# Performance work log

Hardware: AMD Instinct MI355X
Metric: run time of the kernel (lower is better)

The kernel has to match this reference:

```python
import jax, jax.numpy as jnp
import numpy as np

SEQ, BZ, DIM = 2048, 16, 1024
NUM_LANG, DICT_LEN = 16, 32000


def setup_inputs() -> dict:
    key = jax.random.key(0)
    ks = jax.random.split(key, 6)
    x = jax.random.normal(ks[0], (SEQ, BZ, DIM), dtype=jnp.float32)
    # raw language ids live at the tail of the dictionary: dict_len-1-raw in [0, num_lang)
    raw = DICT_LEN - 1 - jax.random.randint(ks[1], (BZ,), 0, NUM_LANG)
    W_base = jax.random.normal(ks[2], (DIM, DIM), dtype=jnp.float32) * (DIM ** -0.5)
    b_base = jax.random.normal(ks[3], (DIM,), dtype=jnp.float32) * 0.02
    W = jax.random.uniform(ks[4], (NUM_LANG, DIM, DIM), dtype=jnp.float32) * (DIM ** -0.5)
    bias = jax.random.uniform(ks[5], (NUM_LANG, DIM), dtype=jnp.float32)
    return {"x": x, "lang_ids": raw, "W_base": W_base, "b_base": b_base,
            "W": W, "bias": bias, "dict_len": DICT_LEN, "num_lang": NUM_LANG}


def reference(x, lang_ids, W_base, b_base, W, bias, dict_len, num_lang):
    # Map raw ids to expert indices in [0, num_lang)
    ids = dict_len - 1 - lang_ids                      # [bz]
    # base_model (nn.Linear): h = x @ W_base.T + b_base
    h = jnp.einsum('sbd,ed->sbe', x, W_base) + b_base  # [seq, bz, dim]
    # The original pads each language group to max group size, runs a batched
    # einsum 'abcd,ade->abce' over languages, then scatters back with per-lang
    # bias. Mathematically each batch column j gets W[lang_j] applied:
    We = W[ids]                                        # [bz, dim, dim]
    out = jnp.einsum('sbd,bde->sbe', h, We) + bias[ids][None, :, :]
    return out
```

## Files before the change

kernel.cpp:

```cpp
#include <hip/hip_runtime.h>
#include <stdint.h>

typedef unsigned short u16;
typedef unsigned int u32;
typedef __bf16 bf16x8 __attribute__((ext_vector_type(8)));
typedef float f32x4 __attribute__((ext_vector_type(4)));

#define SEQ 2048
#define BZ 16
#define DIM 1024

__device__ __forceinline__ u16 f2bf(float f) {
    union { float f; u32 u; } a; a.f = f;
    u32 r = a.u + 0x7FFFu + ((a.u >> 16) & 1u);
    return (u16)(r >> 16);
}
__device__ __forceinline__ float bf2f(u16 u) {
    union { u32 u; float f; } a; a.u = ((u32)u) << 16;
    return a.f;
}

__global__ void transpose_cvt(const float* __restrict__ W,
                              const float* __restrict__ W_base,
                              const int* __restrict__ lang_ids,
                              const int* __restrict__ dict_len,
                              u16* __restrict__ Wt,
                              u16* __restrict__ Wbt)
{
    int z = blockIdx.z;
    const float* S;
    u16* D;
    if (z < BZ) {
        int id = dict_len[0] - 1 - lang_ids[z];
        S = W + (size_t)id * DIM * DIM;
        D = Wbt + (size_t)z * DIM * DIM;
    } else {
        S = W_base;
        D = Wt;
    }
    __shared__ float tile[32][33];
    int tx = threadIdx.x, ty = threadIdx.y;
    int x0 = blockIdx.x * 32, y0 = blockIdx.y * 32;
    #pragma unroll
    for (int i = 0; i < 4; i++)
        tile[ty + 8 * i][tx] = S[(size_t)(y0 + ty + 8 * i) * DIM + x0 + tx];
    __syncthreads();
    #pragma unroll
    for (int i = 0; i < 4; i++)
        D[(size_t)(x0 + ty + 8 * i) * DIM + y0 + tx] = f2bf(tile[tx][ty + 8 * i]);
}

__global__ void bb_kernel(const u16* __restrict__ Wbt,
                          const float* __restrict__ b_base,
                          const float* __restrict__ bias,
                          const int* __restrict__ lang_ids,
                          const int* __restrict__ dict_len,
                          float* __restrict__ bb)
{
    int gw = blockIdx.x * 4 + (threadIdx.x >> 6);
    int b = gw >> 10;
    int f = gw & 1023;
    int lane = threadIdx.x & 63;
    const u16* row = Wbt + ((size_t)b * DIM + f) * DIM;
    float s = 0.f;
    #pragma unroll
    for (int i = 0; i < DIM / 64; i++)
        s += bf2f(row[lane + 64 * i]) * b_base[lane + 64 * i];
    #pragma unroll
    for (int off = 32; off; off >>= 1)
        s += __shfl_xor(s, off, 64);
    if (lane == 0) {
        int id = dict_len[0] - 1 - lang_ids[b];
        bb[b * DIM + f] = s + bias[(size_t)id * DIM + f];
    }
}

__global__ void gemm1_kernel(const u16* __restrict__ Wbt,
                             const u16* __restrict__ Wt,
                             u16* __restrict__ CT)
{
    int b = blockIdx.z;
    int f0 = blockIdx.y * 128;
    int d0 = blockIdx.x * 128;
    const u16* A = Wbt + (size_t)b * DIM * DIM;
    const u16* B = Wt;
    u16* C = CT + (size_t)b * DIM * DIM;

    __shared__ u16 As[128 * 32];
    __shared__ u16 Bs[128 * 32];

    int tid = threadIdx.x;
    int wave = tid >> 6, lane = tid & 63;
    int wm = (wave >> 1) * 64, wn = (wave & 1) * 64;
    int quad = lane >> 4, lr = lane & 15;

    f32x4 acc[4][4];
    #pragma unroll
    for (int i = 0; i < 4; i++)
        #pragma unroll
        for (int j = 0; j < 4; j++)
            #pragma unroll
            for (int e = 0; e < 4; e++) acc[i][j][e] = 0.f;

    int r = tid >> 1, c = (tid & 1) * 16;
    for (int k0 = 0; k0 < DIM; k0 += 32) {
        const uint4* asrc = (const uint4*)(A + (size_t)(f0 + r) * DIM + k0 + c);
        const uint4* bsrc = (const uint4*)(B + (size_t)(d0 + r) * DIM + k0 + c);
        uint4 a0 = asrc[0], a1 = asrc[1];
        uint4 b0 = bsrc[0], b1 = bsrc[1];
        *(uint4*)&As[r * 32 + c] = a0;
        *(uint4*)&As[r * 32 + c + 8] = a1;
        *(uint4*)&Bs[r * 32 + c] = b0;
        *(uint4*)&Bs[r * 32 + c + 8] = b1;
        __syncthreads();
        bf16x8 af[4], bfv[4];
        #pragma unroll
        for (int mt = 0; mt < 4; mt++)
            af[mt] = *(const bf16x8*)&As[(wm + mt * 16 + lr) * 32 + quad * 8];
        #pragma unroll
        for (int nt = 0; nt < 4; nt++)
            bfv[nt] = *(const bf16x8*)&Bs[(wn + nt * 16 + lr) * 32 + quad * 8];
        #pragma unroll
        for (int mt = 0; mt < 4; mt++)
            #pragma unroll
            for (int nt = 0; nt < 4; nt++)
                acc[mt][nt] = __builtin_amdgcn_mfma_f32_16x16x32_bf16(
                    af[mt], bfv[nt], acc[mt][nt], 0, 0, 0);
        __syncthreads();
    }
    #pragma unroll
    for (int mt = 0; mt < 4; mt++) {
        int fr = f0 + wm + mt * 16 + quad * 4;
        #pragma unroll
        for (int nt = 0; nt < 4; nt++) {
            int dc = d0 + wn + nt * 16 + lr;
            #pragma unroll
            for (int rr = 0; rr < 4; rr++)
                C[(size_t)(fr + rr) * DIM + dc] = f2bf(acc[mt][nt][rr]);
        }
    }
}

__global__ void gemm2_kernel(const float* __restrict__ x,
                             const u16* __restrict__ CT,
                             const float* __restrict__ bb,
                             float* __restrict__ out)
{
    int b = blockIdx.z;
    int s0 = blockIdx.y * 128;
    int f0 = blockIdx.x * 128;
    const u16* Bm = CT + (size_t)b * DIM * DIM;

    __shared__ u16 As[128 * 32];
    __shared__ u16 Bs[128 * 32];

    int tid = threadIdx.x;
    int wave = tid >> 6, lane = tid & 63;
    int wm = (wave >> 1) * 64, wn = (wave & 1) * 64;
    int quad = lane >> 4, lr = lane & 15;

    f32x4 acc[4][4];
    #pragma unroll
    for (int i = 0; i < 4; i++)
        #pragma unroll
        for (int j = 0; j < 4; j++)
            #pragma unroll
            for (int e = 0; e < 4; e++) acc[i][j][e] = 0.f;

    int r = tid >> 1, c = (tid & 1) * 16;
    for (int k0 = 0; k0 < DIM; k0 += 32) {
        const float4* asrc = (const float4*)(x + ((size_t)(s0 + r) * BZ + b) * DIM + k0 + c);
        float4 fa = asrc[0], fb = asrc[1], fc = asrc[2], fd = asrc[3];
        const uint4* bsrc = (const uint4*)(Bm + (size_t)(f0 + r) * DIM + k0 + c);
        uint4 b0 = bsrc[0], b1 = bsrc[1];
        u32 u0 = f2bf(fa.x) | ((u32)f2bf(fa.y) << 16);
        u32 u1 = f2bf(fa.z) | ((u32)f2bf(fa.w) << 16);
        u32 u2 = f2bf(fb.x) | ((u32)f2bf(fb.y) << 16);
        u32 u3 = f2bf(fb.z) | ((u32)f2bf(fb.w) << 16);
        u32 u4 = f2bf(fc.x) | ((u32)f2bf(fc.y) << 16);
        u32 u5 = f2bf(fc.z) | ((u32)f2bf(fc.w) << 16);
        u32 u6 = f2bf(fd.x) | ((u32)f2bf(fd.y) << 16);
        u32 u7 = f2bf(fd.z) | ((u32)f2bf(fd.w) << 16);
        *(uint4*)&As[r * 32 + c] = make_uint4(u0, u1, u2, u3);
        *(uint4*)&As[r * 32 + c + 8] = make_uint4(u4, u5, u6, u7);
        *(uint4*)&Bs[r * 32 + c] = b0;
        *(uint4*)&Bs[r * 32 + c + 8] = b1;
        __syncthreads();
        bf16x8 af[4], bfv[4];
        #pragma unroll
        for (int mt = 0; mt < 4; mt++)
            af[mt] = *(const bf16x8*)&As[(wm + mt * 16 + lr) * 32 + quad * 8];
        #pragma unroll
        for (int nt = 0; nt < 4; nt++)
            bfv[nt] = *(const bf16x8*)&Bs[(wn + nt * 16 + lr) * 32 + quad * 8];
        #pragma unroll
        for (int mt = 0; mt < 4; mt++)
            #pragma unroll
            for (int nt = 0; nt < 4; nt++)
                acc[mt][nt] = __builtin_amdgcn_mfma_f32_16x16x32_bf16(
                    af[mt], bfv[nt], acc[mt][nt], 0, 0, 0);
        __syncthreads();
    }
    #pragma unroll
    for (int nt = 0; nt < 4; nt++) {
        int fcol = f0 + wn + nt * 16 + lr;
        float bv = bb[b * DIM + fcol];
        #pragma unroll
        for (int mt = 0; mt < 4; mt++) {
            int sr = s0 + wm + mt * 16 + quad * 4;
            #pragma unroll
            for (int rr = 0; rr < 4; rr++)
                out[((size_t)(sr + rr) * BZ + b) * DIM + fcol] = acc[mt][nt][rr] + bv;
        }
    }
}

extern "C" void kernel_launch(void* const* d_in, const int* in_sizes, int n_in,
                              void* d_out, int out_size, void* d_ws, size_t ws_size,
                              hipStream_t stream)
{
    const float* x        = (const float*)d_in[0];
    const int*   lang_ids = (const int*)d_in[1];
    const float* W_base   = (const float*)d_in[2];
    const float* b_base   = (const float*)d_in[3];
    const float* W        = (const float*)d_in[4];
    const float* bias     = (const float*)d_in[5];
    const int*   dict_len = (const int*)d_in[6];
    float* out = (float*)d_out;

    char* ws = (char*)d_ws;
    u16*  Wt  = (u16*)ws;
    u16*  Wbt = (u16*)(ws + (size_t)(2u << 20));
    u16*  CT  = (u16*)(ws + (size_t)(34u << 20));
    float* bb = (float*)(ws + (size_t)(66u << 20));

    transpose_cvt<<<dim3(32, 32, 17), dim3(32, 8, 1), 0, stream>>>(
        W, W_base, lang_ids, dict_len, Wt, Wbt);
    bb_kernel<<<dim3(4096, 1, 1), 256, 0, stream>>>(
        Wbt, b_base, bias, lang_ids, dict_len, bb);
    gemm1_kernel<<<dim3(8, 8, 16), 256, 0, stream>>>(Wbt, Wt, CT);
    gemm2_kernel<<<dim3(8, 16, 16), 256, 0, stream>>>(x, CT, bb, out);
}
```

Before: 481.5 us.

## Pre-convert x to bf16 and use direct global-to-LDS loads in GEMMs

Adds a pass that converts x to bf16 in a batch-major layout up front. Both GEMM kernels now stage tiles with global_load_lds async copies instead of loading through registers and storing to LDS. This removes the per-tile fp32-to-bf16 conversion inside gemm2, which was repeated for every f-tile block, and the extra register round trip. In exchange it costs an extra 128MB read plus 64MB write pass over x and adds a dependence on how the async LDS loads are ordered relative to the barrier.

```diff
diff --git a/kernel.cpp b/kernel.cpp
--- a/kernel.cpp
+++ b/kernel.cpp
@@ -18,6 +18,28 @@
 __device__ __forceinline__ float bf2f(u16 u) {
     union { u32 u; float f; } a; a.u = ((u32)u) << 16;
     return a.f;
+}
+__device__ __forceinline__ void async16(const u16* g, u16* l) {
+    __builtin_amdgcn_global_load_lds(
+        (const __attribute__((address_space(1))) void*)g,
+        (__attribute__((address_space(3))) void*)l, 16, 0, 0);
+}
+
+__global__ void convert_x(const float* __restrict__ x, u16* __restrict__ xb)
+{
+    int s = blockIdx.x;
+    int t = threadIdx.x;
+    const float4* src = (const float4*)(x + (size_t)s * BZ * DIM);
+    #pragma unroll
+    for (int j = 0; j < 16; j++) {
+        int idx = j * 256 + t;
+        float4 v = src[idx];
+        int e = idx * 4;
+        int b = e >> 10, d = e & 1023;
+        u32 lo = f2bf(v.x) | ((u32)f2bf(v.y) << 16);
+        u32 hi = f2bf(v.z) | ((u32)f2bf(v.w) << 16);
+        *(uint2*)(xb + ((size_t)b * SEQ + s) * DIM + d) = make_uint2(lo, hi);
+    }
 }
 
 __global__ void transpose_cvt(const float* __restrict__ W,
@@ -94,6 +116,17 @@
     int wm = (wave >> 1) * 64, wn = (wave & 1) * 64;
     int quad = lane >> 4, lr = lane & 15;
 
+    int srow = wave * 32 + (lane >> 2);
+    int scol = (lane & 3) * 8;
+    const u16* ga0 = A + (size_t)(f0 + srow) * DIM + scol;
+    const u16* ga1 = ga0 + (size_t)16 * DIM;
+    const u16* gb0 = B + (size_t)(d0 + srow) * DIM + scol;
+    const u16* gb1 = gb0 + (size_t)16 * DIM;
+    u16* la0 = &As[(wave * 32) * 32];
+    u16* la1 = &As[(wave * 32 + 16) * 32];
+    u16* lb0 = &Bs[(wave * 32) * 32];
+    u16* lb1 = &Bs[(wave * 32 + 16) * 32];
+
     f32x4 acc[4][4];
     #pragma unroll
     for (int i = 0; i < 4; i++)
@@ -102,16 +135,10 @@
             #pragma unroll
             for (int e = 0; e < 4; e++) acc[i][j][e] = 0.f;
 
-    int r = tid >> 1, c = (tid & 1) * 16;
     for (int k0 = 0; k0 < DIM; k0 += 32) {
-        const uint4* asrc = (const uint4*)(A + (size_t)(f0 + r) * DIM + k0 + c);
-        const uint4* bsrc = (const uint4*)(B + (size_t)(d0 + r) * DIM + k0 + c);
-        uint4 a0 = asrc[0], a1 = asrc[1];
-        uint4 b0 = bsrc[0], b1 = bsrc[1];
-        *(uint4*)&As[r * 32 + c] = a0;
-        *(uint4*)&As[r * 32 + c + 8] = a1;
-        *(uint4*)&Bs[r * 32 + c] = b0;
-        *(uint4*)&Bs[r * 32 + c + 8] = b1;
+        async16(ga0, la0); async16(ga1, la1);
+        async16(gb0, lb0); async16(gb1, lb1);
+        ga0 += 32; ga1 += 32; gb0 += 32; gb1 += 32;
         __syncthreads();
         bf16x8 af[4], bfv[4];
         #pragma unroll
@@ -141,7 +168,7 @@
     }
 }
 
-__global__ void gemm2_kernel(const float* __restrict__ x,
+__global__ void gemm2_kernel(const u16* __restrict__ xb,
                              const u16* __restrict__ CT,
                              const float* __restrict__ bb,
                              float* __restrict__ out)
@@ -149,6 +176,7 @@
     int b = blockIdx.z;
     int s0 = blockIdx.y * 128;
     int f0 = blockIdx.x * 128;
+    const u16* A = xb + (size_t)b * SEQ * DIM;
     const u16* Bm = CT + (size_t)b * DIM * DIM;
 
     __shared__ u16 As[128 * 32];
@@ -159,6 +187,17 @@
     int wm = (wave >> 1) * 64, wn = (wave & 1) * 64;
     int quad = lane >> 4, lr = lane & 15;
 
+    int srow = wave * 32 + (lane >> 2);
+    int scol = (lane & 3) * 8;
+    const u16* ga0 = A + (size_t)(s0 + srow) * DIM + scol;
+    const u16* ga1 = ga0 + (size_t)16 * DIM;
+    const u16* gb0 = Bm + (size_t)(f0 + srow) * DIM + scol;
+    const u16* gb1 = gb0 + (size_t)16 * DIM;
+    u16* la0 = &As[(wave * 32) * 32];
+    u16* la1 = &As[(wave * 32 + 16) * 32];
+    u16* lb0 = &Bs[(wave * 32) * 32];
+    u16* lb1 = &Bs[(wave * 32 + 16) * 32];
+
     f32x4 acc[4][4];
     #pragma unroll
     for (int i = 0; i < 4; i++)
@@ -167,24 +206,10 @@
             #pragma unroll
             for (int e = 0; e < 4; e++) acc[i][j][e] = 0.f;
 
-    int r = tid >> 1, c = (tid & 1) * 16;
     for (int k0 = 0; k0 < DIM; k0 += 32) {
-        const float4* asrc = (const float4*)(x + ((size_t)(s0 + r) * BZ + b) * DIM + k0 + c);
-        float4 fa = asrc[0], fb = asrc[1], fc = asrc[2], fd = asrc[3];
-        const uint4* bsrc = (const uint4*)(Bm + (size_t)(f0 + r) * DIM + k0 + c);
-        uint4 b0 = bsrc[0], b1 = bsrc[1];
-        u32 u0 = f2bf(fa.x) | ((u32)f2bf(fa.y) << 16);
-        u32 u1 = f2bf(fa.z) | ((u32)f2bf(fa.w) << 16);
-        u32 u2 = f2bf(fb.x) | ((u32)f2bf(fb.y) << 16);
-        u32 u3 = f2bf(fb.z) | ((u32)f2bf(fb.w) << 16);
-        u32 u4 = f2bf(fc.x) | ((u32)f2bf(fc.y) << 16);
-        u32 u5 = f2bf(fc.z) | ((u32)f2bf(fc.w) << 16);
-        u32 u6 = f2bf(fd.x) | ((u32)f2bf(fd.y) << 16);
-        u32 u7 = f2bf(fd.z) | ((u32)f2bf(fd.w) << 16);
-        *(uint4*)&As[r * 32 + c] = make_uint4(u0, u1, u2, u3);
-        *(uint4*)&As[r * 32 + c + 8] = make_uint4(u4, u5, u6, u7);
-        *(uint4*)&Bs[r * 32 + c] = b0;
-        *(uint4*)&Bs[r * 32 + c + 8] = b1;
+        async16(ga0, la0); async16(ga1, la1);
+        async16(gb0, lb0); async16(gb1, lb1);
+        ga0 += 32; ga1 += 32; gb0 += 32; gb1 += 32;
         __syncthreads();
         bf16x8 af[4], bfv[4];
         #pragma unroll
@@ -233,11 +258,13 @@
     u16*  Wbt = (u16*)(ws + (size_t)(2u << 20));
     u16*  CT  = (u16*)(ws + (size_t)(34u << 20));
     float* bb = (float*)(ws + (size_t)(66u << 20));
-
+    u16*  xb  = (u16*)(ws + (size_t)(67u << 20));
+
+    convert_x<<<dim3(SEQ, 1, 1), 256, 0, stream>>>(x, xb);
     transpose_cvt<<<dim3(32, 32, 17), dim3(32, 8, 1), 0, stream>>>(
         W, W_base, lang_ids, dict_len, Wt, Wbt);
     bb_kernel<<<dim3(4096, 1, 1), 256, 0, stream>>>(
         Wbt, b_base, bias, lang_ids, dict_len, bb);
     gemm1_kernel<<<dim3(8, 8, 16), 256, 0, stream>>>(Wbt, Wt, CT);
-    gemm2_kernel<<<dim3(8, 16, 16), 256, 0, stream>>>(x, CT, bb, out);
-}
+    gemm2_kernel<<<dim3(8, 16, 16), 256, 0, stream>>>(xb, CT, bb, out);
+}
```

Measured after the change: 453.6 us. 5.8% less time.
